# Kernel tuning notes

Hardware: AMD Instinct MI355X
Metric: run time of the kernel (lower is better)

Reference implementation:

```python
import jax, jax.numpy as jnp
import numpy as np

E_NODES_C = 50000   # constraints
E_NODES_V = 100000  # variables
N_EDGES = 1600000
EMB = 64
EDGE_NFEATS = 1
N_LAYERS = 2
N_CONVS = 2 * N_LAYERS  # v_to_c and c_to_v per layer
EPS = 1e-5


def setup_inputs() -> dict:
    key = jax.random.key(0)
    ks = jax.random.split(key, 24)
    s = 1.0 / np.sqrt(EMB)
    inp = {
        "constraint_features": jax.random.normal(ks[0], (E_NODES_C, EMB), jnp.float32),
        "variable_features": jax.random.normal(ks[1], (E_NODES_V, EMB), jnp.float32),
        "edge_indices": jnp.stack([
            jax.random.randint(ks[2], (N_EDGES,), 0, E_NODES_C, jnp.int32),
            jax.random.randint(ks[3], (N_EDGES,), 0, E_NODES_V, jnp.int32),
        ]),
        "edge_features": jax.random.normal(ks[4], (N_EDGES, EDGE_NFEATS), jnp.float32),
        # stacked params for the 4 conv blocks
        "Wl": jax.random.normal(ks[5], (N_CONVS, EMB, EMB), jnp.float32) * s,
        "bl": jnp.zeros((N_CONVS, EMB), jnp.float32),
        "We": jax.random.normal(ks[6], (N_CONVS, EMB, EDGE_NFEATS), jnp.float32) * s,
        "Wr": jax.random.normal(ks[7], (N_CONVS, EMB, EMB), jnp.float32) * s,
        "g1": jnp.ones((N_CONVS, EMB), jnp.float32),
        "b1": jnp.zeros((N_CONVS, EMB), jnp.float32),
        "Wf": jax.random.normal(ks[8], (N_CONVS, EMB, EMB), jnp.float32) * s,
        "bf": jnp.zeros((N_CONVS, EMB), jnp.float32),
        "g2": jnp.ones((N_CONVS, EMB), jnp.float32),
        "b2": jnp.zeros((N_CONVS, EMB), jnp.float32),
        "Wo1": jax.random.normal(ks[9], (N_CONVS, EMB, 2 * EMB), jnp.float32) * s,
        "bo1": jnp.zeros((N_CONVS, EMB), jnp.float32),
        "Wo2": jax.random.normal(ks[10], (N_CONVS, EMB, EMB), jnp.float32) * s,
        "bo2": jnp.zeros((N_CONVS, EMB), jnp.float32),
    }
    return inp


def _layer_norm(x, g, b):
    m = jnp.mean(x, axis=-1, keepdims=True)
    v = jnp.mean(jnp.square(x - m), axis=-1, keepdims=True)
    return (x - m) * jax.lax.rsqrt(v + EPS) * g + b


def _conv(k, left, src, dst, ef, right, P):
    # message: Lin(right_i) + Lin_nobias(edge) + Lin_nobias(left_j)
    h = (right[dst] @ P["Wl"][k].T + P["bl"][k]
         + ef @ P["We"][k].T
         + left[src] @ P["Wr"][k].T)                       # [E, emb]
    h = jax.nn.relu(_layer_norm(h, P["g1"][k], P["b1"][k]))
    h = h @ P["Wf"][k].T + P["bf"][k]
    agg = jax.ops.segment_sum(h, dst, num_segments=right.shape[0])  # [N_right, emb]
    z = jnp.concatenate([_layer_norm(agg, P["g2"][k], P["b2"][k]), right], axis=-1)
    return jax.nn.relu(z @ P["Wo1"][k].T + P["bo1"][k]) @ P["Wo2"][k].T + P["bo2"][k]


def reference(constraint_features, variable_features, edge_indices, edge_features,
              Wl, bl, We, Wr, g1, b1, Wf, bf, g2, b2, Wo1, bo1, Wo2, bo2):
    P = dict(Wl=Wl, bl=bl, We=We, Wr=Wr, g1=g1, b1=b1, Wf=Wf, bf=bf,
             g2=g2, b2=b2, Wo1=Wo1, bo1=bo1, Wo2=Wo2, bo2=bo2)
    ci, vi = edge_indices[0], edge_indices[1]
    c, v = constraint_features, variable_features
    for i in range(N_LAYERS):
        # v_to_c: left=variables (src=vi), right=constraints (dst=ci)
        c = c + _conv(2 * i, v, vi, ci, edge_features, c, P)
        # c_to_v: left=constraints (src=ci), right=variables (dst=vi)
        v = v + _conv(2 * i + 1, c, ci, vi, edge_features, v, P)
    return (c, v)
```

## Files before the change

kernel.cpp:

```cpp
#include <hip/hip_runtime.h>

#define EMB   64
#define NCON  50000
#define NVAR  100000
#define NEDGE 1600000
#define EPSLN 1e-5f

#define PADEC (NEDGE + 15 * NCON)
#define PADEV (NEDGE + 15 * NVAR)

#define HCHUNK 12544
#define HSEG   32
#define HCHC   4
#define HCHV   8

typedef _Float16 half2_t __attribute__((ext_vector_type(2)));
typedef _Float16 f16x8  __attribute__((ext_vector_type(8)));
typedef float    f32x2  __attribute__((ext_vector_type(2)));
typedef float    f32x4  __attribute__((ext_vector_type(4)));

template <int CTRL, int RMASK>
__device__ __forceinline__ float dpp_add_f(float x) {
    int m = __builtin_amdgcn_update_dpp(0, __builtin_bit_cast(int, x), CTRL, RMASK, 0xf, true);
    return x + __builtin_bit_cast(float, m);
}
__device__ __forceinline__ float wtotal64(float x) {
    x = dpp_add_f<0x111, 0xf>(x);
    x = dpp_add_f<0x112, 0xf>(x);
    x = dpp_add_f<0x114, 0xf>(x);
    x = dpp_add_f<0x118, 0xf>(x);
    x = dpp_add_f<0x142, 0xa>(x);
    x = dpp_add_f<0x143, 0xc>(x);
    return __builtin_bit_cast(float, __builtin_amdgcn_readlane(__builtin_bit_cast(int, x), 63));
}
template <int CTRL, int RMASK>
__device__ __forceinline__ int dpp_add_i(int x) {
    return x + __builtin_amdgcn_update_dpp(0, x, CTRL, RMASK, 0xf, true);
}
__device__ __forceinline__ int wtotal64_i(int x) {
    x = dpp_add_i<0x111, 0xf>(x);
    x = dpp_add_i<0x112, 0xf>(x);
    x = dpp_add_i<0x114, 0xf>(x);
    x = dpp_add_i<0x118, 0xf>(x);
    x = dpp_add_i<0x142, 0xa>(x);
    x = dpp_add_i<0x143, 0xc>(x);
    return __builtin_amdgcn_readlane(x, 63);
}

__device__ __forceinline__ float dot2f(half2_t a, half2_t b, float c) {
    return __builtin_amdgcn_fdot2(a, b, c, false);
}

__device__ __forceinline__ half2_t hmax2(half2_t a, half2_t b) {
#if defined(__has_builtin) && __has_builtin(__builtin_elementwise_max)
    return __builtin_elementwise_max(a, b);
#else
    half2_t r;
    r.x = a.x > b.x ? a.x : b.x;
    r.y = a.y > b.y ? a.y : b.y;
    return r;
#endif
}

__device__ __forceinline__ float matvec_f16(const _Float16* __restrict__ buf,
                                            const half2_t* __restrict__ wh, float acc) {
    const float4* hp4 = (const float4*)buf;
    float a0 = acc, a1 = 0.0f, a2 = 0.0f, a3 = 0.0f;
#pragma unroll
    for (int j4 = 0; j4 < 8; ++j4) {
        float4 t = hp4[j4];
        a0 = dot2f(wh[4 * j4 + 0], __builtin_bit_cast(half2_t, t.x), a0);
        a1 = dot2f(wh[4 * j4 + 1], __builtin_bit_cast(half2_t, t.y), a1);
        a2 = dot2f(wh[4 * j4 + 2], __builtin_bit_cast(half2_t, t.z), a2);
        a3 = dot2f(wh[4 * j4 + 3], __builtin_bit_cast(half2_t, t.w), a3);
    }
    return (a0 + a1) + (a2 + a3);
}

__device__ __forceinline__ void load_w_f16(const float* __restrict__ W, int stride,
                                           int lane, half2_t* wh) {
#pragma unroll
    for (int j4 = 0; j4 < 16; ++j4) {
        float4 t = *(const float4*)(W + (size_t)lane * stride + j4 * 4);
        wh[2 * j4 + 0] = half2_t{(_Float16)t.x, (_Float16)t.y};
        wh[2 * j4 + 1] = half2_t{(_Float16)t.z, (_Float16)t.w};
    }
}

__device__ __forceinline__ f16x8 cvt8_f16(float4 u, float4 v) {
    f16x8 r;
    r[0] = (_Float16)u.x; r[1] = (_Float16)u.y; r[2] = (_Float16)u.z; r[3] = (_Float16)u.w;
    r[4] = (_Float16)v.x; r[5] = (_Float16)v.y; r[6] = (_Float16)v.z; r[7] = (_Float16)v.w;
    return r;
}


__global__ __launch_bounds__(256) void hist_part_kernel(
        const int* __restrict__ ci, const int* __restrict__ vi,
        int* __restrict__ partC, int* __restrict__ partV, int E) {
    __shared__ int lh[HCHUNK];
    const int seg  = blockIdx.x % HSEG;
    const int cg   = blockIdx.x / HSEG;
    const bool isC = cg < HCHC;
    const int chunk = isC ? cg : cg - HCHC;
    const int base  = chunk * HCHUNK;
    const int* __restrict__ dst = isC ? ci : vi;
    int* __restrict__ part = (isC ? partC : partV) + (size_t)(chunk * HSEG + seg) * HCHUNK;

    int4* l4 = (int4*)lh;
    for (int i = threadIdx.x; i < HCHUNK / 4; i += 256) l4[i] = make_int4(0, 0, 0, 0);
    __syncthreads();

    const int s0 = (int)((long long)seg * E / HSEG);
    const int s1 = (int)((long long)(seg + 1) * E / HSEG);
    for (int i = s0 + threadIdx.x; i < s1; i += 256) {
        const unsigned rel = (unsigned)(dst[i] - base);
        if (rel < (unsigned)HCHUNK) atomicAdd(&lh[rel], 1);
    }
    __syncthreads();
    int4* p4 = (int4*)part;
    for (int i = threadIdx.x; i < HCHUNK / 4; i += 256) p4[i] = l4[i];
}

__global__ __launch_bounds__(256) void hist_reduce_kernel(
        const int* __restrict__ partC, const int* __restrict__ partV,
        int* __restrict__ degC, int* __restrict__ degV) {
    int j = blockIdx.x * blockDim.x + threadIdx.x;
    const int tot = NCON + NVAR;
    for (; j < tot; j += gridDim.x * blockDim.x) {
        if (j < NCON) {
            const int chunk = j / HCHUNK, off = j - chunk * HCHUNK;
            const int* p = partC + (size_t)chunk * HSEG * HCHUNK + off;
            int s = 0;
#pragma unroll
            for (int t = 0; t < HSEG; ++t) s += p[(size_t)t * HCHUNK];
            degC[j] = s;
        } else {
            const int jj = j - NCON;
            const int chunk = jj / HCHUNK, off = jj - chunk * HCHUNK;
            const int* p = partV + (size_t)chunk * HSEG * HCHUNK + off;
            int s = 0;
#pragma unroll
            for (int t = 0; t < HSEG; ++t) s += p[(size_t)t * HCHUNK];
            degV[jj] = s;
        }
    }
}

__global__ __launch_bounds__(256) void hist2_kernel(
        const int* __restrict__ ci, const int* __restrict__ vi,
        int* __restrict__ degC, int* __restrict__ degV, int E) {
    int i = blockIdx.x * blockDim.x + threadIdx.x;
    for (; i < E; i += gridDim.x * blockDim.x) {
        atomicAdd(&degC[ci[i]], 1);
        atomicAdd(&degV[vi[i]], 1);
    }
}

template <bool PAD>
__global__ __launch_bounds__(256) void chunk_sum_kernel(const int* __restrict__ hist,
                                                        int* __restrict__ csum, int N) {
    __shared__ int wpart[4];
    const int base = blockIdx.x * 1024 + threadIdx.x * 4;
    int s = 0;
    if (base + 3 < N) {
        int4 t = *(const int4*)(hist + base);
        if (PAD) s = ((t.x+15)&~15) + ((t.y+15)&~15) + ((t.z+15)&~15) + ((t.w+15)&~15);
        else     s = t.x + t.y + t.z + t.w;
    } else {
#pragma unroll
        for (int j = 0; j < 4; ++j)
            if (base + j < N) { int v = hist[base + j]; s += PAD ? ((v+15)&~15) : v; }
    }
    s = wtotal64_i(s);
    if ((threadIdx.x & 63) == 0) wpart[threadIdx.x >> 6] = s;
    __syncthreads();
    if (threadIdx.x == 0) csum[blockIdx.x] = wpart[0] + wpart[1] + wpart[2] + wpart[3];
}

__global__ void chunk_offsets_kernel(const int* __restrict__ csum, int* __restrict__ coff,
                                     int* __restrict__ rowptr, int nchunk, int N) {
    const int lane = threadIdx.x;
    int carry = 0;
    for (int base = 0; base < nchunk; base += 64) {
        const int i = base + lane;
        int val = (i < nchunk) ? csum[i] : 0;
        int incl = val;
#pragma unroll
        for (int off = 1; off < 64; off <<= 1) {
            int t = __shfl_up(incl, off, 64);
            if (lane >= off) incl += t;
        }
        if (i < nchunk) coff[i] = incl - val + carry;
        carry += __shfl(incl, 63, 64);
    }
    if (lane == 0) rowptr[N] = carry;
}

template <bool PAD>
__global__ __launch_bounds__(256) void chunk_apply_kernel(
        const int* __restrict__ hist, const int* __restrict__ coff,
        int* __restrict__ rowptr, int* __restrict__ cursor, int N) {
    __shared__ int wpart[4];
    const int wv = threadIdx.x >> 6;
    const int lane = threadIdx.x & 63;
    const int base = blockIdx.x * 1024 + threadIdx.x * 4;
    int v0 = 0, v1 = 0, v2 = 0, v3 = 0;
    if (base + 3 < N) {
        int4 t = *(const int4*)(hist + base);
        v0 = t.x; v1 = t.y; v2 = t.z; v3 = t.w;
    } else {
        if (base + 0 < N) v0 = hist[base + 0];
        if (base + 1 < N) v1 = hist[base + 1];
        if (base + 2 < N) v2 = hist[base + 2];
        if (base + 3 < N) v3 = hist[base + 3];
    }
    if (PAD) { v0 = (v0+15)&~15; v1 = (v1+15)&~15; v2 = (v2+15)&~15; v3 = (v3+15)&~15; }
    const int s = v0 + v1 + v2 + v3;
    int incl = s;
#pragma unroll
    for (int off = 1; off < 64; off <<= 1) {
        int t = __shfl_up(incl, off, 64);
        if (lane >= off) incl += t;
    }
    if (lane == 63) wpart[wv] = incl;
    __syncthreads();
    int excl = coff[blockIdx.x] + incl - s;
    for (int w = 0; w < wv; ++w) excl += wpart[w];
    if (base + 0 < N) { rowptr[base + 0] = excl; cursor[base + 0] = excl; excl += v0; }
    if (base + 1 < N) { rowptr[base + 1] = excl; cursor[base + 1] = excl; excl += v1; }
    if (base + 2 < N) { rowptr[base + 2] = excl; cursor[base + 2] = excl; excl += v2; }
    if (base + 3 < N) { rowptr[base + 3] = excl; cursor[base + 3] = excl; excl += v3; }
}

template <int NDST>
__global__ __launch_bounds__(256) void scatter_dir_kernel(
        const int* __restrict__ dst, const int* __restrict__ src,
        const float* __restrict__ ef,
        int* __restrict__ cur, int2* __restrict__ ep, int E) {
    const int rep = blockIdx.x & 7;
    const int stride = (gridDim.x >> 3) * blockDim.x;
    int i = (blockIdx.x >> 3) * blockDim.x + threadIdx.x;
    for (; i < E; i += stride) {
        const int d = dst[i];
        const int b = (int)(((long long)d * 8) / NDST);
        if (b == rep) {
            const int slot = atomicAdd(&cur[d], 1);
            ep[slot] = make_int2(src[i], __float_as_int(ef[i]));
        }
    }
}


__global__ __launch_bounds__(256, 3) void lin2_kernel(
        const float* __restrict__ XR, const float* __restrict__ WR,
        const float* __restrict__ bR, _Float16* __restrict__ YR, int NR,
        const float* __restrict__ XL, const float* __restrict__ WL,
        _Float16* __restrict__ YL, int NL, int nbR) {
    const int wv   = threadIdx.x >> 6;
    const int lane = threadIdx.x & 63;
    const int col  = lane & 15;
    const int kgrp = lane >> 4;
    const bool isR = (int)blockIdx.x < nbR;
    const float* X = isR ? XR : XL;
    const float* W = isR ? WR : WL;
    _Float16* Y    = isR ? YR : YL;
    const int N    = isR ? NR : NL;
    const int b0   = isR ? 0 : nbR;
    const int nb   = isR ? nbR : (gridDim.x - nbR);

    f16x8 bf[4][2];
#pragma unroll
    for (int ct = 0; ct < 4; ++ct)
#pragma unroll
        for (int kc = 0; kc < 2; ++kc) {
            const float* wrow = W + (size_t)(ct * 16 + col) * EMB + kc * 32 + kgrp * 8;
            bf[ct][kc] = cvt8_f16(*(const float4*)wrow, *(const float4*)(wrow + 4));
        }
    float bias[4];
#pragma unroll
    for (int ct = 0; ct < 4; ++ct) bias[ct] = isR ? bR[ct * 16 + col] : 0.0f;

    const int ntile = (N + 15) >> 4;
    const int nW = nb * 4;
    for (int t = ((int)blockIdx.x - b0) * 4 + wv; t < ntile; t += nW) {
        const int n0 = t << 4;
        const int srow = min(n0 + col, N - 1);
        const float* xrow = X + (size_t)srow * EMB + kgrp * 8;
        const float4 x0 = *(const float4*)(xrow);
        const float4 x1 = *(const float4*)(xrow + 4);
        const float4 x2 = *(const float4*)(xrow + 32);
        const float4 x3 = *(const float4*)(xrow + 36);
        const f16x8 a0 = cvt8_f16(x0, x1);
        const f16x8 a1 = cvt8_f16(x2, x3);
        f32x4 acc[4];
#pragma unroll
        for (int ct = 0; ct < 4; ++ct) {
            acc[ct] = __builtin_amdgcn_mfma_f32_16x16x32_f16(
                a0, bf[ct][0], (f32x4){0.0f, 0.0f, 0.0f, 0.0f}, 0, 0, 0);
            acc[ct] = __builtin_amdgcn_mfma_f32_16x16x32_f16(
                a1, bf[ct][1], acc[ct], 0, 0, 0);
        }
#pragma unroll
        for (int r = 0; r < 4; ++r) {
            const int n = n0 + (kgrp << 2) + r;
            if (n < N) {
                _Float16* yrow = Y + (size_t)n * EMB + col;
#pragma unroll
                for (int ct = 0; ct < 4; ++ct)
                    yrow[ct * 16] = (_Float16)(acc[ct][r] + bias[ct]);
            }
        }
    }
}


__global__ __launch_bounds__(256, 4) void edge_abar_kernel(
        const int* __restrict__ rp16, const int* __restrict__ deg,
        const int2* __restrict__ ep,
        const _Float16* __restrict__ RL, const _Float16* __restrict__ LL,
        const float* __restrict__ We, const float* __restrict__ g1,
        const float* __restrict__ b1, _Float16* __restrict__ ABAR, int Nr) {
    __shared__ __align__(16) float tbuf[4][16][68];
    const int wv   = threadIdx.x >> 6;
    const int lane = threadIdx.x & 63;
    const int col  = lane & 15;
    const int quad = lane >> 4;
    const int kb   = quad * 8;

    half2_t weh[8], gkh[8], bkh[8];
#pragma unroll
    for (int j = 0; j < 4; ++j) {
        weh[j]     = half2_t{(_Float16)We[kb + 2*j],      (_Float16)We[kb + 2*j + 1]};
        weh[4 + j] = half2_t{(_Float16)We[kb + 32 + 2*j], (_Float16)We[kb + 32 + 2*j + 1]};
        gkh[j]     = half2_t{(_Float16)g1[kb + 2*j],      (_Float16)g1[kb + 2*j + 1]};
        gkh[4 + j] = half2_t{(_Float16)g1[kb + 32 + 2*j], (_Float16)g1[kb + 32 + 2*j + 1]};
        bkh[j]     = half2_t{(_Float16)b1[kb + 2*j],      (_Float16)b1[kb + 2*j + 1]};
        bkh[4 + j] = half2_t{(_Float16)b1[kb + 32 + 2*j], (_Float16)b1[kb + 32 + 2*j + 1]};
    }

    const int nW = gridDim.x * 4;
    int n = blockIdx.x * 4 + wv;
    int pg0 = rp16[n] >> 4;
    int pg1 = rp16[n + 1] >> 4;
    int pdn = deg[n];

    bool livN = false; float fN = 0.0f;
    f16x8 llaN = {}, llbN = {};
    auto issue_group = [&](int gbase, int cnt) {
        livN = col < cnt;
        int2 p = ep[(gbase << 4) + col];
        const int s2 = livN ? p.x : 0;
        fN = livN ? __int_as_float(p.y) : 0.0f;
        llaN = *(const f16x8*)(LL + (size_t)s2 * EMB + kb);
        llbN = *(const f16x8*)(LL + (size_t)s2 * EMB + kb + 32);
    };
    if (pg0 < pg1) issue_group(pg0, pdn);

    while (true) {
        const int g0 = pg0, g1e = pg1, dn = pdn;
        const int nn = n + nW;
        const bool hasNext = nn < Nr;
        if (hasNext) {
            pg0 = rp16[nn] >> 4;
            pg1 = rp16[nn + 1] >> 4;
            pdn = deg[nn];
        }

        half2_t rl2[8];
        *(f16x8*)&rl2[0] = *(const f16x8*)(RL + (size_t)n * EMB + kb);
        *(f16x8*)&rl2[4] = *(const f16x8*)(RL + (size_t)n * EMB + kb + 32);

        f32x2 acc2[8];
#pragma unroll
        for (int j = 0; j < 8; ++j) acc2[j] = f32x2{0.0f, 0.0f};

        bool didNext = false;
        for (int g = g0; g < g1e; ++g) {
            const bool liv = livN;
            const float f = fN;
            half2_t h2[8];
            *(f16x8*)&h2[0] = llaN;
            *(f16x8*)&h2[4] = llbN;
            if (g + 1 < g1e) {
                issue_group(g + 1, dn - ((g + 1 - g0) << 4));
            } else if (hasNext && pg0 < pg1) {
                issue_group(pg0, pdn);
                didNext = true;
            }
            const _Float16 fh = (_Float16)f;
            const half2_t f2 = half2_t{fh, fh};
            const half2_t one2 = half2_t{(_Float16)1.0f, (_Float16)1.0f};
            float ps = 0.0f, pq = 0.0f;
#pragma unroll
            for (int j = 0; j < 8; ++j) {
                h2[j] = (h2[j] + rl2[j]) + f2 * weh[j];
                ps = dot2f(h2[j], one2, ps);
                pq = dot2f(h2[j], h2[j], pq);
            }
            ps += __shfl_xor(ps, 16, 64); ps += __shfl_xor(ps, 32, 64);
            pq += __shfl_xor(pq, 16, 64); pq += __shfl_xor(pq, 32, 64);
            const float mean = ps * (1.0f / EMB);
            const float var  = pq * (1.0f / EMB) - mean * mean;
            const float rs   = rsqrtf(var + EPSLN);
            const _Float16 rsh = (_Float16)rs;
            const _Float16 mnh = (_Float16)mean;
            const half2_t rs2 = half2_t{rsh, rsh};
            const half2_t mn2 = half2_t{mnh, mnh};
            const half2_t z2  = half2_t{(_Float16)0.0f, (_Float16)0.0f};
            if (liv) {
#pragma unroll
                for (int j = 0; j < 8; ++j) {
                    const half2_t sc = gkh[j] * rs2;
                    half2_t a = (h2[j] - mn2) * sc + bkh[j];
                    a = hmax2(a, z2);
                    f32x2 cv; cv.x = (float)a.x; cv.y = (float)a.y;
                    acc2[j] += cv;
                }
            }
        }

        float* tb = &tbuf[wv][col][0];
        *(float4*)(tb + kb)      = make_float4(acc2[0].x, acc2[0].y, acc2[1].x, acc2[1].y);
        *(float4*)(tb + kb + 4)  = make_float4(acc2[2].x, acc2[2].y, acc2[3].x, acc2[3].y);
        *(float4*)(tb + kb + 32) = make_float4(acc2[4].x, acc2[4].y, acc2[5].x, acc2[5].y);
        *(float4*)(tb + kb + 36) = make_float4(acc2[6].x, acc2[6].y, acc2[7].x, acc2[7].y);
        float t0[16];
#pragma unroll
        for (int c2 = 0; c2 < 16; ++c2) t0[c2] = tbuf[wv][c2][lane];
        const float s01 = (t0[0] + t0[1]) + (t0[2] + t0[3]);
        const float s23 = (t0[4] + t0[5]) + (t0[6] + t0[7]);
        const float s45 = (t0[8] + t0[9]) + (t0[10] + t0[11]);
        const float s67 = (t0[12] + t0[13]) + (t0[14] + t0[15]);
        ABAR[(size_t)n * EMB + lane] = (_Float16)((s01 + s23) + (s45 + s67));

        if (!hasNext) break;
        if (!didNext && pg0 < pg1) issue_group(pg0, pdn);
        n = nn;
    }
}


__global__ __launch_bounds__(256, 4) void edge_csr_kernel(
        const int* __restrict__ rowptr, const int2* __restrict__ ep,
        const _Float16* __restrict__ RL, const _Float16* __restrict__ LL,
        const float* __restrict__ Wecol, const float* __restrict__ g1,
        const float* __restrict__ b1,
        _Float16* __restrict__ ABAR, int Nr) {
    const int lane = threadIdx.x & 63;
    const float we  = Wecol[lane];
    const float g   = g1[lane];
    const float bb  = b1[lane];
    const int nW = gridDim.x * 4;
    for (int n = blockIdx.x * 4 + (threadIdx.x >> 6); n < Nr; n += nW) {
        const int beg = rowptr[n];
        const int end = rowptr[n + 1];
        const float rl = (float)RL[(size_t)n * EMB + lane];
        float acc = 0.0f;
        for (int idx = beg; idx < end; ++idx) {
            const int2 p = ep[idx];
            const float f = __int_as_float(p.y);
            float h = rl + (float)LL[(size_t)p.x * EMB + lane] + f * we;
            const float s1 = wtotal64(h);
            const float s2 = wtotal64(h * h);
            const float m   = s1 * (1.0f / EMB);
            const float var = s2 * (1.0f / EMB) - m * m;
            acc += fmaxf((h - m) * rsqrtf(var + EPSLN) * g + bb, 0.0f);
        }
        ABAR[(size_t)n * EMB + lane] = (_Float16)acc;
    }
}


__global__ __launch_bounds__(256, 1) void out_kernel(
        const _Float16* __restrict__ ABAR, const int* __restrict__ deg,
        float* __restrict__ right,
        const float* __restrict__ g2, const float* __restrict__ b2,
        const float* __restrict__ Wf, const float* __restrict__ bfp,
        const float* __restrict__ Wo1, const float* __restrict__ Wo2,
        const float* __restrict__ bo1, const float* __restrict__ bo2, int N) {
    __shared__ __align__(16) _Float16 abuf[4][EMB];
    __shared__ __align__(16) _Float16 zbuf[4][EMB];
    __shared__ __align__(16) _Float16 rbuf[4][EMB];
    __shared__ __align__(16) _Float16 obuf[4][EMB];
    const int wv = threadIdx.x >> 6;
    const int lane = threadIdx.x & 63;
    half2_t whF[32], wh1[32], whB[32], wh2[32];
    load_w_f16(Wf, EMB, lane, whF);
    load_w_f16(Wo1, 2 * EMB, lane, wh1);
    load_w_f16(Wo1 + EMB, 2 * EMB, lane, whB);
    load_w_f16(Wo2, EMB, lane, wh2);
    const float bfv  = bfp[lane];
    const float g    = g2[lane];
    const float bb   = b2[lane];
    const float bo1v = bo1[lane];
    const float bo2v = bo2[lane];
    const int nW = gridDim.x * 4;
    for (int n = blockIdx.x * 4 + wv; n < N; n += nW) {
        abuf[wv][lane] = ABAR[(size_t)n * EMB + lane];
        const int dn = deg[n];
        const float rf = right[(size_t)n * EMB + lane];
        const float a = matvec_f16(abuf[wv], whF, (float)dn * bfv);
        const float s1 = wtotal64(a);
        const float s2 = wtotal64(a * a);
        const float m   = s1 * (1.0f / EMB);
        const float var = s2 * (1.0f / EMB) - m * m;
        const float z = (a - m) * rsqrtf(var + EPSLN) * g + bb;
        zbuf[wv][lane] = (_Float16)z;
        rbuf[wv][lane] = (_Float16)rf;
        float acc = matvec_f16(zbuf[wv], wh1, bo1v);
        acc = matvec_f16(rbuf[wv], whB, acc);
        obuf[wv][lane] = (_Float16)fmaxf(acc, 0.0f);
        float acc2 = matvec_f16(obuf[wv], wh2, bo2v);
        right[(size_t)n * EMB + lane] = rf + acc2;
    }
}

extern "C" void kernel_launch(void* const* d_in, const int* in_sizes, int n_in,
                              void* d_out, int out_size, void* d_ws, size_t ws_size,
                              hipStream_t stream) {
    const float* cf  = (const float*)d_in[0];
    const float* vfp = (const float*)d_in[1];
    const int*   ei  = (const int*)d_in[2];
    const float* ef  = (const float*)d_in[3];
    const float* Wl  = (const float*)d_in[4];
    const float* bl  = (const float*)d_in[5];
    const float* We  = (const float*)d_in[6];
    const float* Wr  = (const float*)d_in[7];
    const float* g1  = (const float*)d_in[8];
    const float* b1  = (const float*)d_in[9];
    const float* Wf  = (const float*)d_in[10];
    const float* bfp = (const float*)d_in[11];
    const float* g2  = (const float*)d_in[12];
    const float* b2  = (const float*)d_in[13];
    const float* Wo1 = (const float*)d_in[14];
    const float* bo1 = (const float*)d_in[15];
    const float* Wo2 = (const float*)d_in[16];
    const float* bo2 = (const float*)d_in[17];

    float* c = (float*)d_out;
    float* v = c + (size_t)NCON * EMB;
    (void)hipMemcpyAsync(c, cf,  (size_t)NCON * EMB * sizeof(float), hipMemcpyDeviceToDevice, stream);
    (void)hipMemcpyAsync(v, vfp, (size_t)NVAR * EMB * sizeof(float), hipMemcpyDeviceToDevice, stream);

    float* wsf = (float*)d_ws;
    size_t off = 0;
    _Float16* AGG = (_Float16*)(wsf + off); off += (size_t)NVAR * EMB / 2;
    _Float16* RL  = (_Float16*)(wsf + off); off += (size_t)NVAR * EMB / 2;
    _Float16* LL  = (_Float16*)(wsf + off); off += (size_t)NVAR * EMB / 2;
    int* degC  = (int*)(wsf + off); off += NCON;
    int* degV  = (int*)(wsf + off); off += NVAR;
    int* rp16C = (int*)(wsf + off); off += NCON + 4;
    int* curC  = (int*)(wsf + off); off += NCON;
    int* rp16V = (int*)(wsf + off); off += NVAR + 4;
    int* curV  = (int*)(wsf + off); off += NVAR;
    int* csumC = (int*)(wsf + off); off += 128;
    int* coffC = (int*)(wsf + off); off += 128;
    int* csumV = (int*)(wsf + off); off += 128;
    int* coffV = (int*)(wsf + off); off += 128;
    size_t off_edges = off;
    int2* epC = (int2*)(wsf + off); off += (size_t)2 * PADEC;
    int2* epV = (int2*)(wsf + off); off += (size_t)2 * PADEV;
    const bool use_mfma = ws_size >= off * sizeof(float);
    int* partC = (int*)(wsf + off); off += (size_t)HCHC * HSEG * HCHUNK;
    int* partV = (int*)(wsf + off); off += (size_t)HCHV * HSEG * HCHUNK;
    const bool use_ldshist = use_mfma && ws_size >= off * sizeof(float);
    if (!use_mfma) {
        off = off_edges;
        epC = (int2*)(wsf + off); off += (size_t)2 * NEDGE;
        epV = (int2*)(wsf + off); off += (size_t)2 * NEDGE;
    }

    const int* ci = ei;
    const int* vi = ei + NEDGE;

    const dim3 blk(256);
    const int NB = 2048;
    const int NBL = 1536;
    const int nchC = (NCON + 1023) / 1024;
    const int nchV = (NVAR + 1023) / 1024;

    if (use_ldshist) {
        hist_part_kernel<<<(HCHC + HCHV) * HSEG, blk, 0, stream>>>(ci, vi, partC, partV, NEDGE);
        hist_reduce_kernel<<<640, blk, 0, stream>>>(partC, partV, degC, degV);
    } else {
        (void)hipMemsetAsync(degC, 0, NCON * sizeof(int), stream);
        (void)hipMemsetAsync(degV, 0, NVAR * sizeof(int), stream);
        hist2_kernel<<<1024, blk, 0, stream>>>(ci, vi, degC, degV, NEDGE);
    }
    if (use_mfma) {
        chunk_sum_kernel<true><<<nchC, blk, 0, stream>>>(degC, csumC, NCON);
        chunk_sum_kernel<true><<<nchV, blk, 0, stream>>>(degV, csumV, NVAR);
        chunk_offsets_kernel<<<1, 64, 0, stream>>>(csumC, coffC, rp16C, nchC, NCON);
        chunk_offsets_kernel<<<1, 64, 0, stream>>>(csumV, coffV, rp16V, nchV, NVAR);
        chunk_apply_kernel<true><<<nchC, blk, 0, stream>>>(degC, coffC, rp16C, curC, NCON);
        chunk_apply_kernel<true><<<nchV, blk, 0, stream>>>(degV, coffV, rp16V, curV, NVAR);
    } else {
        chunk_sum_kernel<false><<<nchC, blk, 0, stream>>>(degC, csumC, NCON);
        chunk_sum_kernel<false><<<nchV, blk, 0, stream>>>(degV, csumV, NVAR);
        chunk_offsets_kernel<<<1, 64, 0, stream>>>(csumC, coffC, rp16C, nchC, NCON);
        chunk_offsets_kernel<<<1, 64, 0, stream>>>(csumV, coffV, rp16V, nchV, NVAR);
        chunk_apply_kernel<false><<<nchC, blk, 0, stream>>>(degC, coffC, rp16C, curC, NCON);
        chunk_apply_kernel<false><<<nchV, blk, 0, stream>>>(degV, coffV, rp16V, curV, NVAR);
    }
    scatter_dir_kernel<NCON><<<2048, blk, 0, stream>>>(ci, vi, ef, curC, epC, NEDGE);
    scatter_dir_kernel<NVAR><<<2048, blk, 0, stream>>>(vi, ci, ef, curV, epV, NEDGE);

    for (int k = 0; k < 4; ++k) {
        const bool v2c = ((k & 1) == 0);
        float* right   = v2c ? c : v;
        float* left    = v2c ? v : c;
        const int Nr   = v2c ? NCON : NVAR;
        const int Nl   = v2c ? NVAR : NCON;
        const int nbR  = v2c ? NBL / 3 : 2 * NBL / 3;
        const int* degR = v2c ? degC : degV;

        lin2_kernel<<<NBL, blk, 0, stream>>>(
            right, Wl + (size_t)k * EMB * EMB, bl + (size_t)k * EMB, RL, Nr,
            left,  Wr + (size_t)k * EMB * EMB, LL, Nl, nbR);

        if (use_mfma) {
            edge_abar_kernel<<<NB, blk, 0, stream>>>(
                v2c ? rp16C : rp16V, degR, v2c ? epC : epV,
                RL, LL, We + (size_t)k * EMB,
                g1 + (size_t)k * EMB, b1 + (size_t)k * EMB,
                AGG, Nr);
        } else {
            edge_csr_kernel<<<NB, blk, 0, stream>>>(
                v2c ? rp16C : rp16V, v2c ? epC : epV,
                RL, LL, We + (size_t)k * EMB,
                g1 + (size_t)k * EMB, b1 + (size_t)k * EMB,
                AGG, Nr);
        }
        out_kernel<<<NB, blk, 0, stream>>>(AGG, degR, right,
                                           g2 + (size_t)k * EMB, b2 + (size_t)k * EMB,
                                           Wf + (size_t)k * EMB * EMB,
                                           bfp + (size_t)k * EMB,
                                           Wo1 + (size_t)k * EMB * 2 * EMB,
                                           Wo2 + (size_t)k * EMB * EMB,
                                           bo1 + (size_t)k * EMB, bo2 + (size_t)k * EMB,
                                           Nr);
    }
}
```

Baseline: 1.123 ms.

## Rewrite node output MLP with 16-row MFMA tiles instead of per-node matvecs

The output kernel now processes 16 nodes per wavefront as a tile and uses 16x16x32 f16 MFMA instructions for the Wf, Wo1 and Wo2 projections, with weights held in registers as B fragments. LayerNorm is computed with cross-lane shuffles, and intermediates are staged through padded LDS tiles. This removes scalar per-node matvec loops and LDS round trips per row. It assumes N is a multiple of 16, which holds for both node counts (50000 and 100000), and changes the memory access pattern for writing back `right`.

Measured after the change: 980.7 us. -12.6%, faster.

```diff
diff --git a/kernel.cpp b/kernel.cpp
--- a/kernel.cpp
+++ b/kernel.cpp
@@ -479,40 +479,123 @@
         const float* __restrict__ Wf, const float* __restrict__ bfp,
         const float* __restrict__ Wo1, const float* __restrict__ Wo2,
         const float* __restrict__ bo1, const float* __restrict__ bo2, int N) {
-    __shared__ __align__(16) _Float16 abuf[4][EMB];
-    __shared__ __align__(16) _Float16 zbuf[4][EMB];
-    __shared__ __align__(16) _Float16 rbuf[4][EMB];
-    __shared__ __align__(16) _Float16 obuf[4][EMB];
-    const int wv = threadIdx.x >> 6;
+    __shared__ __align__(16) _Float16 zt[4][16][72];
+    __shared__ __align__(16) _Float16 ot[4][16][72];
+    const int wv   = threadIdx.x >> 6;
     const int lane = threadIdx.x & 63;
-    half2_t whF[32], wh1[32], whB[32], wh2[32];
-    load_w_f16(Wf, EMB, lane, whF);
-    load_w_f16(Wo1, 2 * EMB, lane, wh1);
-    load_w_f16(Wo1 + EMB, 2 * EMB, lane, whB);
-    load_w_f16(Wo2, EMB, lane, wh2);
-    const float bfv  = bfp[lane];
-    const float g    = g2[lane];
-    const float bb   = b2[lane];
-    const float bo1v = bo1[lane];
-    const float bo2v = bo2[lane];
+    const int col  = lane & 15;
+    const int kgrp = lane >> 4;
+
+    f16x8 bF[4][2], b1a[4][2], b1b[4][2], b2f[4][2];
+#pragma unroll
+    for (int ct = 0; ct < 4; ++ct)
+#pragma unroll
+        for (int kc = 0; kc < 2; ++kc) {
+            const int row = ct * 16 + col;
+            const int ko  = kc * 32 + kgrp * 8;
+            const float* wf = Wf  + (size_t)row * EMB + ko;
+            const float* w1 = Wo1 + (size_t)row * 2 * EMB + ko;
+            const float* w2 = Wo2 + (size_t)row * EMB + ko;
+            bF[ct][kc]  = cvt8_f16(*(const float4*)wf, *(const float4*)(wf + 4));
+            b1a[ct][kc] = cvt8_f16(*(const float4*)w1, *(const float4*)(w1 + 4));
+            b1b[ct][kc] = cvt8_f16(*(const float4*)(w1 + EMB), *(const float4*)(w1 + EMB + 4));
+            b2f[ct][kc] = cvt8_f16(*(const float4*)w2, *(const float4*)(w2 + 4));
+        }
+    float bfc[4], gc[4], bbc[4], bo1c[4], bo2c[4];
+#pragma unroll
+    for (int ct = 0; ct < 4; ++ct) {
+        const int cd = ct * 16 + col;
+        bfc[ct]  = bfp[cd];
+        gc[ct]   = g2[cd];
+        bbc[ct]  = b2[cd];
+        bo1c[ct] = bo1[cd];
+        bo2c[ct] = bo2[cd];
+    }
+
+    const int ntile = N >> 4;
     const int nW = gridDim.x * 4;
-    for (int n = blockIdx.x * 4 + wv; n < N; n += nW) {
-        abuf[wv][lane] = ABAR[(size_t)n * EMB + lane];
-        const int dn = deg[n];
-        const float rf = right[(size_t)n * EMB + lane];
-        const float a = matvec_f16(abuf[wv], whF, (float)dn * bfv);
-        const float s1 = wtotal64(a);
-        const float s2 = wtotal64(a * a);
-        const float m   = s1 * (1.0f / EMB);
-        const float var = s2 * (1.0f / EMB) - m * m;
-        const float z = (a - m) * rsqrtf(var + EPSLN) * g + bb;
-        zbuf[wv][lane] = (_Float16)z;
-        rbuf[wv][lane] = (_Float16)rf;
-        float acc = matvec_f16(zbuf[wv], wh1, bo1v);
-        acc = matvec_f16(rbuf[wv], whB, acc);
-        obuf[wv][lane] = (_Float16)fmaxf(acc, 0.0f);
-        float acc2 = matvec_f16(obuf[wv], wh2, bo2v);
-        right[(size_t)n * EMB + lane] = rf + acc2;
+    for (int t = blockIdx.x * 4 + wv; t < ntile; t += nW) {
+        const int n0 = t << 4;
+        const _Float16* arow = ABAR + (size_t)(n0 + col) * EMB + kgrp * 8;
+        const f16x8 aA0 = *(const f16x8*)(arow);
+        const f16x8 aA1 = *(const f16x8*)(arow + 32);
+        f32x4 acc[4];
+#pragma unroll
+        for (int ct = 0; ct < 4; ++ct) {
+            acc[ct] = __builtin_amdgcn_mfma_f32_16x16x32_f16(
+                aA0, bF[ct][0], (f32x4){0.0f, 0.0f, 0.0f, 0.0f}, 0, 0, 0);
+            acc[ct] = __builtin_amdgcn_mfma_f32_16x16x32_f16(
+                aA1, bF[ct][1], acc[ct], 0, 0, 0);
+        }
+        float dnr[4];
+#pragma unroll
+        for (int r = 0; r < 4; ++r) dnr[r] = (float)deg[n0 + (kgrp << 2) + r];
+#pragma unroll
+        for (int r = 0; r < 4; ++r) {
+            float s1 = 0.0f, s2 = 0.0f;
+#pragma unroll
+            for (int ct = 0; ct < 4; ++ct) {
+                const float a = acc[ct][r] + dnr[r] * bfc[ct];
+                acc[ct][r] = a;
+                s1 += a; s2 += a * a;
+            }
+            s1 += __shfl_xor(s1, 1, 64); s2 += __shfl_xor(s2, 1, 64);
+            s1 += __shfl_xor(s1, 2, 64); s2 += __shfl_xor(s2, 2, 64);
+            s1 += __shfl_xor(s1, 4, 64); s2 += __shfl_xor(s2, 4, 64);
+            s1 += __shfl_xor(s1, 8, 64); s2 += __shfl_xor(s2, 8, 64);
+            const float mean = s1 * (1.0f / EMB);
+            const float var  = s2 * (1.0f / EMB) - mean * mean;
+            const float rs   = rsqrtf(var + EPSLN);
+            const int zr = (kgrp << 2) + r;
+#pragma unroll
+            for (int ct = 0; ct < 4; ++ct)
+                zt[wv][zr][ct * 16 + col] =
+                    (_Float16)((acc[ct][r] - mean) * rs * gc[ct] + bbc[ct]);
+        }
+        const _Float16* zrow = &zt[wv][col][kgrp * 8];
+        const f16x8 zA0 = *(const f16x8*)(zrow);
+        const f16x8 zA1 = *(const f16x8*)(zrow + 32);
+        const float* rrow = right + (size_t)(n0 + col) * EMB + kgrp * 8;
+        const f16x8 rA0 = cvt8_f16(*(const float4*)(rrow), *(const float4*)(rrow + 4));
+        const f16x8 rA1 = cvt8_f16(*(const float4*)(rrow + 32), *(const float4*)(rrow + 36));
+        f32x4 acc3[4];
+#pragma unroll
+        for (int ct = 0; ct < 4; ++ct) {
+            acc3[ct] = __builtin_amdgcn_mfma_f32_16x16x32_f16(
+                zA0, b1a[ct][0], (f32x4){0.0f, 0.0f, 0.0f, 0.0f}, 0, 0, 0);
+            acc3[ct] = __builtin_amdgcn_mfma_f32_16x16x32_f16(
+                zA1, b1a[ct][1], acc3[ct], 0, 0, 0);
+            acc3[ct] = __builtin_amdgcn_mfma_f32_16x16x32_f16(
+                rA0, b1b[ct][0], acc3[ct], 0, 0, 0);
+            acc3[ct] = __builtin_amdgcn_mfma_f32_16x16x32_f16(
+                rA1, b1b[ct][1], acc3[ct], 0, 0, 0);
+        }
+#pragma unroll
+        for (int r = 0; r < 4; ++r) {
+            const int orr = (kgrp << 2) + r;
+#pragma unroll
+            for (int ct = 0; ct < 4; ++ct)
+                ot[wv][orr][ct * 16 + col] =
+                    (_Float16)fmaxf(acc3[ct][r] + bo1c[ct], 0.0f);
+        }
+        const _Float16* orow = &ot[wv][col][kgrp * 8];
+        const f16x8 oA0 = *(const f16x8*)(orow);
+        const f16x8 oA1 = *(const f16x8*)(orow + 32);
+        f32x4 acc4[4];
+#pragma unroll
+        for (int ct = 0; ct < 4; ++ct) {
+            acc4[ct] = __builtin_amdgcn_mfma_f32_16x16x32_f16(
+                oA0, b2f[ct][0], (f32x4){0.0f, 0.0f, 0.0f, 0.0f}, 0, 0, 0);
+            acc4[ct] = __builtin_amdgcn_mfma_f32_16x16x32_f16(
+                oA1, b2f[ct][1], acc4[ct], 0, 0, 0);
+        }
+#pragma unroll
+        for (int r = 0; r < 4; ++r) {
+            float* rr = right + (size_t)(n0 + (kgrp << 2) + r) * EMB + col;
+#pragma unroll
+            for (int ct = 0; ct < 4; ++ct)
+                rr[ct * 16] += acc4[ct][r] + bo2c[ct];
+        }
     }
 }
 
```
